# Kernel optimization log

Hardware: AMD Instinct MI355X
Metric: run time of the kernel (lower is better)

The kernel has to match this reference:

```python
import jax, jax.numpy as jnp
import numpy as np

D_MODEL = 768
H = 12
D_K = D_MODEL // H
B = 2
S = 2048
NEG = -1e9


def setup_inputs() -> dict:
    key = jax.random.key(0)
    ks = jax.random.split(key, 12)
    scale = 1.0 / np.sqrt(D_MODEL)
    inp = {
        "q": jax.random.normal(ks[0], (B, S, D_MODEL), jnp.float32),
        "k": jax.random.normal(ks[1], (B, S, D_MODEL), jnp.float32),
        "v": jax.random.normal(ks[2], (B, S, D_MODEL), jnp.float32),
        "mask": jax.random.randint(ks[3], (B, 1, S, S), 0, 2, jnp.int32),
        "Wq": jax.random.normal(ks[4], (D_MODEL, D_MODEL), jnp.float32) * scale,
        "bq": jnp.zeros((D_MODEL,), jnp.float32),
        "Wk": jax.random.normal(ks[5], (D_MODEL, D_MODEL), jnp.float32) * scale,
        "bk": jnp.zeros((D_MODEL,), jnp.float32),
        "Wv": jax.random.normal(ks[6], (D_MODEL, D_MODEL), jnp.float32) * scale,
        "bv": jnp.zeros((D_MODEL,), jnp.float32),
        "Wo": jax.random.normal(ks[7], (D_MODEL, D_MODEL), jnp.float32) * scale,
        "bo": jnp.zeros((D_MODEL,), jnp.float32),
    }
    return inp


def _split_heads(x):
    # [B, S, D] -> [B, H, S, D_K]
    b, s, _ = x.shape
    return x.reshape(b, s, H, D_K).transpose(0, 2, 1, 3)


def reference(q, k, v, mask, Wq, bq, Wk, bk, Wv, bv, Wo, bo):
    # torch Linear: x @ W.T + b
    query = _split_heads(q @ Wq.T + bq)
    key_ = _split_heads(k @ Wk.T + bk)
    value = _split_heads(v @ Wv.T + bv)

    scores = jnp.einsum("bhqd,bhkd->bhqk", query, key_) / np.sqrt(D_K)
    scores = jnp.where(mask == 0, NEG, scores)
    attn = jax.nn.softmax(scores, axis=-1)  # dropout p=0.0 -> identity

    x = jnp.einsum("bhqk,bhkd->bhqd", attn, value)
    x = x.transpose(0, 2, 1, 3).reshape(q.shape[0], -1, D_MODEL)
    return x @ Wo.T + bo
```

## Files before the change

### kernel.cpp

```cpp
#include <hip/hip_runtime.h>
#include <math.h>

#define DMODEL 768
#define NHEAD 12
#define DKDIM 64
#define BB 2
#define SS 2048
#define MROWS (BB * SS)
#define WELEM (DMODEL * DMODEL)
#define MWORDS (SS / 64)
#define NIT (SS / 64)

typedef unsigned short bf16_t;
typedef __attribute__((ext_vector_type(8))) short s8;
typedef __attribute__((ext_vector_type(4))) float f4;

#define MFMA(a, b, c) __builtin_amdgcn_mfma_f32_16x16x32_bf16((a), (b), (c), 0, 0, 0)

__device__ __forceinline__ bf16_t f2bf(float f) {
    unsigned u = __float_as_uint(f);
    u += 0x7fffu + ((u >> 16) & 1u);
    return (bf16_t)(u >> 16);
}
__device__ __forceinline__ unsigned cvtpk2(float a, float b) {
    unsigned r;
    asm("v_cvt_pk_bf16_f32 %0, %1, %2" : "=v"(r) : "v"(a), "v"(b));
    return r;
}
__device__ __forceinline__ s8 ldfrag(const bf16_t* p) {
    union { uint4 u; s8 s; } x;
    x.u = *(const uint4*)p;
    return x.s;
}
__device__ __forceinline__ void gload16(const bf16_t* g, bf16_t* l) {
    __builtin_amdgcn_global_load_lds(
        (__attribute__((address_space(1))) void*)g,
        (__attribute__((address_space(3))) void*)l,
        16, 0, 0);
}

__device__ __forceinline__ void ld_stage(const bf16_t* p, uint4& u0, uint4& u1) {
    u0 = *(const uint4*)p;
    u1 = *(const uint4*)(p + 8);
}

__global__ void cvt_weights(const float* __restrict__ W0, const float* __restrict__ W1,
                            const float* __restrict__ W2, const float* __restrict__ W3,
                            bf16_t* __restrict__ dst)
{
    const float* src = (blockIdx.y == 0) ? W0 : (blockIdx.y == 1) ? W1
                     : (blockIdx.y == 2) ? W2 : W3;
    bf16_t* d = dst + (size_t)blockIdx.y * WELEM;
    const int i = (blockIdx.x * 256 + threadIdx.x) * 4;
    const float4 v = *(const float4*)(src + i);
    ushort4 h;
    h.x = f2bf(v.x); h.y = f2bf(v.y); h.z = f2bf(v.z); h.w = f2bf(v.w);
    *(ushort4*)(d + i) = h;
}

__global__ __launch_bounds__(256) void cvt_inputs(
    const float* __restrict__ A0, const float* __restrict__ A1,
    const float* __restrict__ A2, bf16_t* __restrict__ dst)
{
    const float* src = (blockIdx.y == 0) ? A0 : (blockIdx.y == 1) ? A1 : A2;
    bf16_t* d = dst + (size_t)blockIdx.y * MROWS * DMODEL;
    const int i = (blockIdx.x * 256 + threadIdx.x) * 4;
    const float4 v = *(const float4*)(src + i);
    ushort4 h;
    h.x = f2bf(v.x); h.y = f2bf(v.y); h.z = f2bf(v.z); h.w = f2bf(v.w);
    *(ushort4*)(d + i) = h;
}

__global__ __launch_bounds__(256) void mask_to_bits(
    const int* __restrict__ mask, unsigned long long* __restrict__ mbits)
{
    const size_t gid = (size_t)blockIdx.x * 256 + threadIdx.x;
    const int m = mask[gid];
    const unsigned long long bal = __ballot(m != 0);
    if ((threadIdx.x & 63) == 0) mbits[gid >> 6] = bal;
}

__global__ __launch_bounds__(256) void gemm_qkv(
    const bf16_t* __restrict__ A0, const bf16_t* __restrict__ A1, const bf16_t* __restrict__ A2,
    const bf16_t* __restrict__ W0, const bf16_t* __restrict__ W1, const bf16_t* __restrict__ W2,
    const float* __restrict__ bias0, const float* __restrict__ bias1, const float* __restrict__ bias2,
    bf16_t* __restrict__ C0, bf16_t* __restrict__ C1, bf16_t* __restrict__ C2,
    float sc0, float sc1, float sc2)
{
    __shared__ uint4 As4[128 * 4];
    __shared__ uint4 Bs4[128 * 4];

    const int z = blockIdx.z;
    const bf16_t* A    = (z == 0) ? A0 : (z == 1) ? A1 : A2;
    const bf16_t* W    = (z == 0) ? W0 : (z == 1) ? W1 : W2;
    const float*  bias = (z == 0) ? bias0 : (z == 1) ? bias1 : bias2;
    bf16_t*       C    = (z == 0) ? C0 : (z == 1) ? C1 : C2;
    const float   sc   = (z == 0) ? sc0 : (z == 1) ? sc1 : sc2;

    const int tid  = threadIdx.x;
    const int lane = tid & 63;
    const int w    = tid >> 6;
    const int wm   = w & 1;
    const int wn   = w >> 1;
    const int l15  = lane & 15;
    const int quad = lane >> 4;
    const int m0   = blockIdx.y * 128;
    const int n0   = blockIdx.x * 128;

    const int r0 = tid >> 2,         s0 = (tid & 3) ^ (r0 & 3);
    const int r1 = 64 + (tid >> 2),  s1 = (tid & 3) ^ (r1 & 3);
    const bf16_t* aS0 = A + (size_t)(m0 + r0) * DMODEL + s0 * 8;
    const bf16_t* aS1 = A + (size_t)(m0 + r1) * DMODEL + s1 * 8;
    const bf16_t* wS0 = W + (size_t)(n0 + r0) * DMODEL + s0 * 8;
    const bf16_t* wS1 = W + (size_t)(n0 + r1) * DMODEL + s1 * 8;
    bf16_t* aD0 = (bf16_t*)As4 + w * 512;
    bf16_t* aD1 = (bf16_t*)As4 + 2048 + w * 512;
    bf16_t* bD0 = (bf16_t*)Bs4 + w * 512;
    bf16_t* bD1 = (bf16_t*)Bs4 + 2048 + w * 512;

    f4 acc[4][4];
    #pragma unroll
    for (int i = 0; i < 4; i++)
        #pragma unroll
        for (int j = 0; j < 4; j++)
            acc[i][j] = (f4){0.f, 0.f, 0.f, 0.f};

    for (int k0 = 0; k0 < DMODEL; k0 += 32) {
        __syncthreads();
        gload16(aS0 + k0, aD0);
        gload16(aS1 + k0, aD1);
        gload16(wS0 + k0, bD0);
        gload16(wS1 + k0, bD1);
        __syncthreads();

        s8 af[4], bf[4];
        #pragma unroll
        for (int t = 0; t < 4; t++) {
            const int ar = wm * 64 + t * 16 + l15;
            const int br = wn * 64 + t * 16 + l15;
            union { uint4 u; s8 s; } xa, xb;
            xa.u = As4[ar * 4 + (quad ^ (ar & 3))];
            xb.u = Bs4[br * 4 + (quad ^ (br & 3))];
            af[t] = xa.s;
            bf[t] = xb.s;
        }
        #pragma unroll
        for (int mt = 0; mt < 4; mt++)
            #pragma unroll
            for (int nt = 0; nt < 4; nt++)
                acc[mt][nt] = MFMA(af[mt], bf[nt], acc[mt][nt]);
    }

    #pragma unroll
    for (int mt = 0; mt < 4; mt++) {
        #pragma unroll
        for (int nt = 0; nt < 4; nt++) {
            const int col = n0 + wn * 64 + nt * 16 + l15;
            const float bb = bias[col];
            #pragma unroll
            for (int reg = 0; reg < 4; reg++) {
                const int row = m0 + wm * 64 + mt * 16 + quad * 4 + reg;
                C[(size_t)row * DMODEL + col] = f2bf((acc[mt][nt][reg] + bb) * sc);
            }
        }
    }
}

__global__ __launch_bounds__(256) void gemm_out(
    const bf16_t* __restrict__ A, const bf16_t* __restrict__ W,
    const float* __restrict__ bias, float* __restrict__ C)
{
    __shared__ uint4 As4[64 * 4];
    __shared__ uint4 Bs4[128 * 4];

    const int tid  = threadIdx.x;
    const int lane = tid & 63;
    const int w    = tid >> 6;
    const int l15  = lane & 15;
    const int quad = lane >> 4;
    const int m0   = blockIdx.y * 64;
    const int n0   = blockIdx.x * 128;

    const int srow  = tid >> 1;
    const int shalf = tid & 1;
    const int sw    = srow & 3;
    const int arow  = (tid < 128) ? srow : 0;

    const bf16_t* aptr = A + (size_t)(m0 + arow) * DMODEL + shalf * 16;
    const bf16_t* wptr = W + (size_t)(n0 + srow) * DMODEL + shalf * 16;

    f4 acc[4][2];
    #pragma unroll
    for (int i = 0; i < 4; i++)
        #pragma unroll
        for (int j = 0; j < 2; j++)
            acc[i][j] = (f4){0.f, 0.f, 0.f, 0.f};

    for (int k0 = 0; k0 < DMODEL; k0 += 32) {
        uint4 au0, au1, bu0, bu1;
        if (tid < 128) ld_stage(aptr + k0, au0, au1);
        ld_stage(wptr + k0, bu0, bu1);
        __syncthreads();
        if (tid < 128) {
            As4[srow * 4 + ((shalf * 2 + 0) ^ sw)] = au0;
            As4[srow * 4 + ((shalf * 2 + 1) ^ sw)] = au1;
        }
        Bs4[srow * 4 + ((shalf * 2 + 0) ^ sw)] = bu0;
        Bs4[srow * 4 + ((shalf * 2 + 1) ^ sw)] = bu1;
        __syncthreads();

        s8 af[4], bf[2];
        #pragma unroll
        for (int t = 0; t < 4; t++) {
            const int ar = t * 16 + l15;
            union { uint4 u; s8 s; } xa;
            xa.u = As4[ar * 4 + (quad ^ (ar & 3))];
            af[t] = xa.s;
        }
        #pragma unroll
        for (int nt = 0; nt < 2; nt++) {
            const int br = w * 32 + nt * 16 + l15;
            union { uint4 u; s8 s; } xb;
            xb.u = Bs4[br * 4 + (quad ^ (br & 3))];
            bf[nt] = xb.s;
        }
        #pragma unroll
        for (int mt = 0; mt < 4; mt++)
            #pragma unroll
            for (int nt = 0; nt < 2; nt++)
                acc[mt][nt] = MFMA(af[mt], bf[nt], acc[mt][nt]);
    }

    #pragma unroll
    for (int mt = 0; mt < 4; mt++) {
        #pragma unroll
        for (int nt = 0; nt < 2; nt++) {
            const int col = n0 + w * 32 + nt * 16 + l15;
            const float bb = bias[col];
            #pragma unroll
            for (int reg = 0; reg < 4; reg++) {
                const int row = m0 + mt * 16 + quad * 4 + reg;
                C[(size_t)row * DMODEL + col] = acc[mt][nt][reg] + bb;
            }
        }
    }
}

__global__ __launch_bounds__(256) void attn_mfma(
    const bf16_t* __restrict__ Q, const bf16_t* __restrict__ K,
    const bf16_t* __restrict__ V, const unsigned long long* __restrict__ mbits,
    bf16_t* __restrict__ O)
{
    __shared__ unsigned Vs[2][64][36];

    const int tid  = threadIdx.x;
    const int lane = tid & 63;
    const int w    = tid >> 6;
    const int l15  = lane & 15;
    const int quad = lane >> 4;
    const int q0   = blockIdx.x * 64;
    const int h    = blockIdx.y;
    const int b    = blockIdx.z;
    const size_t base = ((size_t)b * SS) * DMODEL + (size_t)h * DKDIM;

    const bf16_t* qrow = Q + base + (size_t)(q0 + w * 16 + l15) * DMODEL + quad * 8;
    const s8 qf0 = ldfrag(qrow);
    const s8 qf1 = ldfrag(qrow + 32);

    f4 oacc[4];
    #pragma unroll
    for (int i = 0; i < 4; i++) oacc[i] = (f4){0.f, 0.f, 0.f, 0.f};
    float l_part = 0.0f;

    const int kp  = tid & 31;
    const int oct = tid >> 5;
    const bf16_t* vbase = V + base + (size_t)(2 * kp) * DMODEL + oct * 8;
    const bf16_t* kbase = K + base + (size_t)l15 * DMODEL + quad * 8;

    const unsigned long long* mbase =
        mbits + ((size_t)b * SS + (q0 + w * 16 + l15)) * MWORDS;

    const int sA  = l15 + (((2 * quad) & 3) << 4);
    const int sB  = l15 + (((2 * quad + 1) & 3) << 4);
    const bool hiQ = (quad & 2) != 0;

    uint4 va = *(const uint4*)(vbase);
    uint4 vb = *(const uint4*)(vbase + DMODEL);
    {
        const unsigned short* pa = (const unsigned short*)&va;
        const unsigned short* pb = (const unsigned short*)&vb;
        #pragma unroll
        for (int i = 0; i < 8; i++)
            Vs[0][oct * 8 + i][kp] = (unsigned)pa[i] | ((unsigned)pb[i] << 16);
    }
    va = *(const uint4*)(vbase + (size_t)64 * DMODEL);
    vb = *(const uint4*)(vbase + (size_t)64 * DMODEL + DMODEL);

    s8 kf0[4], kf1[4];
    unsigned long long mw;
    #pragma unroll
    for (int nt = 0; nt < 4; nt++) {
        const bf16_t* krow = kbase + (size_t)(nt * 16) * DMODEL;
        kf0[nt] = ldfrag(krow);
        kf1[nt] = ldfrag(krow + 32);
    }
    mw = mbase[0];

    __syncthreads();

    for (int it = 0; it < NIT; ++it) {
        const int k0  = it * 64;
        const int cur = it & 1;

        if (it + 1 < NIT) {
            const unsigned short* pa = (const unsigned short*)&va;
            const unsigned short* pb = (const unsigned short*)&vb;
            #pragma unroll
            for (int i = 0; i < 8; i++)
                Vs[cur ^ 1][oct * 8 + i][kp] = (unsigned)pa[i] | ((unsigned)pb[i] << 16);
            if (it + 2 < NIT) {
                va = *(const uint4*)(vbase + (size_t)(k0 + 128) * DMODEL);
                vb = *(const uint4*)(vbase + (size_t)(k0 + 128) * DMODEL + DMODEL);
            }
        }

        f4 sacc[4];
        __builtin_amdgcn_s_setprio(1);
        #pragma unroll
        for (int nt = 0; nt < 4; nt++) {
            f4 zz = {0.f, 0.f, 0.f, 0.f};
            zz = MFMA(kf0[nt], qf0, zz);
            zz = MFMA(kf1[nt], qf1, zz);
            sacc[nt] = zz;
        }
        __builtin_amdgcn_s_setprio(0);

        const unsigned long long mwc = mw;
        if (it + 1 < NIT) {
            #pragma unroll
            for (int nt = 0; nt < 4; nt++) {
                const bf16_t* krow = kbase + (size_t)(k0 + 64 + nt * 16) * DMODEL;
                kf0[nt] = ldfrag(krow);
                kf1[nt] = ldfrag(krow + 32);
            }
            mw = mbase[it + 1];
        }

        const unsigned ml = ((unsigned)mwc) >> (quad * 4);
        const unsigned mh = ((unsigned)(mwc >> 32)) >> (quad * 4);
        unsigned wlo[4], whi[4];
        #pragma unroll
        for (int nt = 0; nt < 4; nt++) {
            const unsigned mm = (nt & 2) ? mh : ml;
            const int shft = (nt & 1) * 16;
            const float p0 = ((mm >> (shft + 0)) & 1u) ? __builtin_exp2f(sacc[nt][0]) : 0.0f;
            const float p1 = ((mm >> (shft + 1)) & 1u) ? __builtin_exp2f(sacc[nt][1]) : 0.0f;
            const float p2 = ((mm >> (shft + 2)) & 1u) ? __builtin_exp2f(sacc[nt][2]) : 0.0f;
            const float p3 = ((mm >> (shft + 3)) & 1u) ? __builtin_exp2f(sacc[nt][3]) : 0.0f;
            l_part += (p0 + p1) + (p2 + p3);
            wlo[nt] = cvtpk2(p0, p1);
            whi[nt] = cvtpk2(p2, p3);
        }

        #pragma unroll
        for (int kt = 0; kt < 2; kt++) {
            const unsigned a0 = (unsigned)__shfl((int)wlo[2 * kt],     sA, 64);
            const unsigned a1 = (unsigned)__shfl((int)wlo[2 * kt + 1], sA, 64);
            const unsigned b0 = (unsigned)__shfl((int)whi[2 * kt],     sA, 64);
            const unsigned b1 = (unsigned)__shfl((int)whi[2 * kt + 1], sA, 64);
            const unsigned c0 = (unsigned)__shfl((int)wlo[2 * kt],     sB, 64);
            const unsigned c1 = (unsigned)__shfl((int)wlo[2 * kt + 1], sB, 64);
            const unsigned d0 = (unsigned)__shfl((int)whi[2 * kt],     sB, 64);
            const unsigned d1 = (unsigned)__shfl((int)whi[2 * kt + 1], sB, 64);
            union { uint4 u; s8 s; } pf;
            pf.u.x = hiQ ? a1 : a0;
            pf.u.y = hiQ ? b1 : b0;
            pf.u.z = hiQ ? c1 : c0;
            pf.u.w = hiQ ? d1 : d0;

            __builtin_amdgcn_s_setprio(1);
            #pragma unroll
            for (int dt = 0; dt < 4; dt++) {
                union { uint4 u; s8 s; } vf;
                vf.u = *(const uint4*)&Vs[cur][dt * 16 + l15][kt * 16 + quad * 4];
                oacc[dt] = MFMA(pf.s, vf.s, oacc[dt]);
            }
            __builtin_amdgcn_s_setprio(0);
        }

        __syncthreads();
    }

    l_part += __shfl_xor(l_part, 16, 64);
    l_part += __shfl_xor(l_part, 32, 64);
    const float inv = 1.0f / l_part;

    #pragma unroll
    for (int reg = 0; reg < 4; reg++) {
        const float invq = __shfl(inv, (quad << 4) + quad * 4 + reg, 64);
        const size_t row = q0 + w * 16 + quad * 4 + reg;
        #pragma unroll
        for (int dt = 0; dt < 4; dt++) {
            O[base + row * DMODEL + dt * 16 + l15] = f2bf(oacc[dt][reg] * invq);
        }
    }
}

extern "C" void kernel_launch(void* const* d_in, const int* in_sizes, int n_in,
                              void* d_out, int out_size, void* d_ws, size_t ws_size,
                              hipStream_t stream)
{
    const float* q    = (const float*)d_in[0];
    const float* k    = (const float*)d_in[1];
    const float* v    = (const float*)d_in[2];
    const int*   mask = (const int*)  d_in[3];
    const float* Wq   = (const float*)d_in[4];
    const float* bq   = (const float*)d_in[5];
    const float* Wk   = (const float*)d_in[6];
    const float* bk   = (const float*)d_in[7];
    const float* Wv   = (const float*)d_in[8];
    const float* bv   = (const float*)d_in[9];
    const float* Wo   = (const float*)d_in[10];
    const float* bo   = (const float*)d_in[11];
    float* out = (float*)d_out;

    bf16_t* wsb = (bf16_t*)d_ws;
    const size_t plane = (size_t)MROWS * DMODEL;
    bf16_t* Qp  = wsb;
    bf16_t* Kp  = wsb + plane;
    bf16_t* Vp  = wsb + 2 * plane;
    bf16_t* Ctx = wsb + 3 * plane;
    bf16_t* Wqb = wsb + 4 * plane;
    bf16_t* Wkb = Wqb + WELEM;
    bf16_t* Wvb = Wkb + WELEM;
    bf16_t* Wob = Wvb + WELEM;
    bf16_t* Abf = Wob + WELEM;
    unsigned long long* mbits = (unsigned long long*)(Abf + 3 * plane);

    cvt_weights<<<dim3(WELEM / 1024, 4), 256, 0, stream>>>(Wq, Wk, Wv, Wo, Wqb);
    cvt_inputs<<<dim3((int)(plane / 1024), 3), 256, 0, stream>>>(q, k, v, Abf);
    mask_to_bits<<<dim3((BB * SS * SS) / 256), 256, 0, stream>>>(mask, mbits);

    gemm_qkv<<<dim3(DMODEL / 128, MROWS / 128, 3), 256, 0, stream>>>(
        Abf, Abf + plane, Abf + 2 * plane, Wqb, Wkb, Wvb, bq, bk, bv,
        Qp, Kp, Vp, 0.125f * 1.44269504f, 1.0f, 1.0f);

    attn_mfma<<<dim3(SS / 64, NHEAD, BB), 256, 0, stream>>>(Qp, Kp, Vp, mbits, Ctx);

    gemm_out<<<dim3(DMODEL / 128, MROWS / 64), 256, 0, stream>>>(Ctx, Wob, bo, out);
}
```

Baseline: 307.6 us.

## Write V transposed from projection GEMM and split attention keys across two wave groups

The V projection epilogue now writes V in a per-head transposed layout [B,H,DK,S], so the attention kernel can load V fragments straight from global memory into registers. That removes the LDS staging and repacking of V and the per-iteration block barrier. The attention block grows to 512 threads: two groups of four waves each process half of the key range, and their partial outputs and row sums are combined through shared memory at the end. This doubles the waves working on each query tile, at the cost of strided 4-byte stores in the V epilogue and a final reduction step.

```diff
diff --git a/kernel.cpp b/kernel.cpp
--- a/kernel.cpp
+++ b/kernel.cpp
@@ -9,7 +9,8 @@
 #define MROWS (BB * SS)
 #define WELEM (DMODEL * DMODEL)
 #define MWORDS (SS / 64)
-#define NIT (SS / 64)
+#define KCHUNK (SS / 2)
+#define NITH (KCHUNK / 64)
 
 typedef unsigned short bf16_t;
 typedef __attribute__((ext_vector_type(8))) short s8;
@@ -21,6 +22,9 @@
     unsigned u = __float_as_uint(f);
     u += 0x7fffu + ((u >> 16) & 1u);
     return (bf16_t)(u >> 16);
+}
+__device__ __forceinline__ unsigned pack2(float a, float b) {
+    return (unsigned)f2bf(a) | ((unsigned)f2bf(b) << 16);
 }
 __device__ __forceinline__ unsigned cvtpk2(float a, float b) {
     unsigned r;
@@ -153,14 +157,28 @@
 
     #pragma unroll
     for (int mt = 0; mt < 4; mt++) {
+        const int grow = m0 + wm * 64 + mt * 16 + quad * 4;
         #pragma unroll
         for (int nt = 0; nt < 4; nt++) {
             const int col = n0 + wn * 64 + nt * 16 + l15;
             const float bb = bias[col];
-            #pragma unroll
-            for (int reg = 0; reg < 4; reg++) {
-                const int row = m0 + wm * 64 + mt * 16 + quad * 4 + reg;
-                C[(size_t)row * DMODEL + col] = f2bf((acc[mt][nt][reg] + bb) * sc);
+            if (z == 2) {
+                const int bidx = grow >> 11;
+                const int sr   = grow & (SS - 1);
+                const float v0 = acc[mt][nt][0] + bb;
+                const float v1 = acc[mt][nt][1] + bb;
+                const float v2 = acc[mt][nt][2] + bb;
+                const float v3 = acc[mt][nt][3] + bb;
+                unsigned* dst = (unsigned*)(C +
+                    ((size_t)(bidx * NHEAD + (col >> 6)) * DKDIM + (col & 63)) * SS + sr);
+                dst[0] = pack2(v0, v1);
+                dst[1] = pack2(v2, v3);
+            } else {
+                #pragma unroll
+                for (int reg = 0; reg < 4; reg++) {
+                    C[(size_t)(grow + reg) * DMODEL + col] =
+                        f2bf((acc[mt][nt][reg] + bb) * sc);
+                }
             }
         }
     }
@@ -246,24 +264,29 @@
     }
 }
 
-__global__ __launch_bounds__(256) void attn_mfma(
+__global__ __launch_bounds__(512) void attn_mfma(
     const bf16_t* __restrict__ Q, const bf16_t* __restrict__ K,
-    const bf16_t* __restrict__ V, const unsigned long long* __restrict__ mbits,
+    const bf16_t* __restrict__ Vt, const unsigned long long* __restrict__ mbits,
     bf16_t* __restrict__ O)
 {
-    __shared__ unsigned Vs[2][64][36];
+    __shared__ float Osh[4][16][68];
+    __shared__ float Lsh[4][16];
 
     const int tid  = threadIdx.x;
     const int lane = tid & 63;
     const int w    = tid >> 6;
+    const int wq   = w & 3;
+    const int ws   = w >> 2;
     const int l15  = lane & 15;
     const int quad = lane >> 4;
     const int q0   = blockIdx.x * 64;
     const int h    = blockIdx.y;
     const int b    = blockIdx.z;
+    const int ks   = ws * KCHUNK;
     const size_t base = ((size_t)b * SS) * DMODEL + (size_t)h * DKDIM;
-
-    const bf16_t* qrow = Q + base + (size_t)(q0 + w * 16 + l15) * DMODEL + quad * 8;
+    const bf16_t* vtb = Vt + (size_t)(b * NHEAD + h) * DKDIM * SS;
+
+    const bf16_t* qrow = Q + base + (size_t)(q0 + wq * 16 + l15) * DMODEL + quad * 8;
     const s8 qf0 = ldfrag(qrow);
     const s8 qf1 = ldfrag(qrow + 32);
 
@@ -272,57 +295,33 @@
     for (int i = 0; i < 4; i++) oacc[i] = (f4){0.f, 0.f, 0.f, 0.f};
     float l_part = 0.0f;
 
-    const int kp  = tid & 31;
-    const int oct = tid >> 5;
-    const bf16_t* vbase = V + base + (size_t)(2 * kp) * DMODEL + oct * 8;
     const bf16_t* kbase = K + base + (size_t)l15 * DMODEL + quad * 8;
+    const bf16_t* vfb = vtb + (size_t)l15 * SS + ks + quad * 8;
 
     const unsigned long long* mbase =
-        mbits + ((size_t)b * SS + (q0 + w * 16 + l15)) * MWORDS;
+        mbits + ((size_t)b * SS + (q0 + wq * 16 + l15)) * MWORDS + (ks >> 6);
 
     const int sA  = l15 + (((2 * quad) & 3) << 4);
     const int sB  = l15 + (((2 * quad + 1) & 3) << 4);
     const bool hiQ = (quad & 2) != 0;
 
-    uint4 va = *(const uint4*)(vbase);
-    uint4 vb = *(const uint4*)(vbase + DMODEL);
-    {
-        const unsigned short* pa = (const unsigned short*)&va;
-        const unsigned short* pb = (const unsigned short*)&vb;
-        #pragma unroll
-        for (int i = 0; i < 8; i++)
-            Vs[0][oct * 8 + i][kp] = (unsigned)pa[i] | ((unsigned)pb[i] << 16);
-    }
-    va = *(const uint4*)(vbase + (size_t)64 * DMODEL);
-    vb = *(const uint4*)(vbase + (size_t)64 * DMODEL + DMODEL);
-
-    s8 kf0[4], kf1[4];
+    s8 kf0[4], kf1[4], vf0[4], vf1[4];
     unsigned long long mw;
     #pragma unroll
     for (int nt = 0; nt < 4; nt++) {
-        const bf16_t* krow = kbase + (size_t)(nt * 16) * DMODEL;
+        const bf16_t* krow = kbase + (size_t)(ks + nt * 16) * DMODEL;
         kf0[nt] = ldfrag(krow);
         kf1[nt] = ldfrag(krow + 32);
     }
     mw = mbase[0];
-
-    __syncthreads();
-
-    for (int it = 0; it < NIT; ++it) {
-        const int k0  = it * 64;
-        const int cur = it & 1;
-
-        if (it + 1 < NIT) {
-            const unsigned short* pa = (const unsigned short*)&va;
-            const unsigned short* pb = (const unsigned short*)&vb;
-            #pragma unroll
-            for (int i = 0; i < 8; i++)
-                Vs[cur ^ 1][oct * 8 + i][kp] = (unsigned)pa[i] | ((unsigned)pb[i] << 16);
-            if (it + 2 < NIT) {
-                va = *(const uint4*)(vbase + (size_t)(k0 + 128) * DMODEL);
-                vb = *(const uint4*)(vbase + (size_t)(k0 + 128) * DMODEL + DMODEL);
-            }
-        }
+    #pragma unroll
+    for (int dt = 0; dt < 4; dt++) {
+        vf0[dt] = ldfrag(vfb + (size_t)(dt * 16) * SS);
+        vf1[dt] = ldfrag(vfb + (size_t)(dt * 16) * SS + 32);
+    }
+
+    for (int it = 0; it < NITH; ++it) {
+        const int k0 = ks + it * 64;
 
         f4 sacc[4];
         __builtin_amdgcn_s_setprio(1);
@@ -336,7 +335,7 @@
         __builtin_amdgcn_s_setprio(0);
 
         const unsigned long long mwc = mw;
-        if (it + 1 < NIT) {
+        if (it + 1 < NITH) {
             #pragma unroll
             for (int nt = 0; nt < 4; nt++) {
                 const bf16_t* krow = kbase + (size_t)(k0 + 64 + nt * 16) * DMODEL;
@@ -379,29 +378,56 @@
             pf.u.w = hiQ ? d1 : d0;
 
             __builtin_amdgcn_s_setprio(1);
+            if (kt == 0) {
+                #pragma unroll
+                for (int dt = 0; dt < 4; dt++)
+                    oacc[dt] = MFMA(pf.s, vf0[dt], oacc[dt]);
+            } else {
+                #pragma unroll
+                for (int dt = 0; dt < 4; dt++)
+                    oacc[dt] = MFMA(pf.s, vf1[dt], oacc[dt]);
+            }
+            __builtin_amdgcn_s_setprio(0);
+        }
+
+        if (it + 1 < NITH) {
             #pragma unroll
             for (int dt = 0; dt < 4; dt++) {
-                union { uint4 u; s8 s; } vf;
-                vf.u = *(const uint4*)&Vs[cur][dt * 16 + l15][kt * 16 + quad * 4];
-                oacc[dt] = MFMA(pf.s, vf.s, oacc[dt]);
-            }
-            __builtin_amdgcn_s_setprio(0);
-        }
-
-        __syncthreads();
+                vf0[dt] = ldfrag(vfb + (size_t)(dt * 16) * SS + (it + 1) * 64);
+                vf1[dt] = ldfrag(vfb + (size_t)(dt * 16) * SS + (it + 1) * 64 + 32);
+            }
+        }
     }
 
     l_part += __shfl_xor(l_part, 16, 64);
     l_part += __shfl_xor(l_part, 32, 64);
-    const float inv = 1.0f / l_part;
-
-    #pragma unroll
-    for (int reg = 0; reg < 4; reg++) {
-        const float invq = __shfl(inv, (quad << 4) + quad * 4 + reg, 64);
-        const size_t row = q0 + w * 16 + quad * 4 + reg;
-        #pragma unroll
-        for (int dt = 0; dt < 4; dt++) {
-            O[base + row * DMODEL + dt * 16 + l15] = f2bf(oacc[dt][reg] * invq);
+
+    if (ws == 1) {
+        #pragma unroll
+        for (int dt = 0; dt < 4; dt++)
+            #pragma unroll
+            for (int reg = 0; reg < 4; reg++)
+                Osh[wq][quad * 4 + reg][dt * 16 + l15] = oacc[dt][reg];
+        if (quad == 0) Lsh[wq][l15] = l_part;
+    }
+    __syncthreads();
+
+    if (ws == 0) {
+        const float inv = 1.0f / (l_part + Lsh[wq][l15]);
+        #pragma unroll
+        for (int dt = 0; dt < 4; dt++)
+            #pragma unroll
+            for (int reg = 0; reg < 4; reg++)
+                oacc[dt][reg] += Osh[wq][quad * 4 + reg][dt * 16 + l15];
+
+        #pragma unroll
+        for (int reg = 0; reg < 4; reg++) {
+            const float invq = __shfl(inv, (quad << 4) + quad * 4 + reg, 64);
+            const size_t row = q0 + wq * 16 + quad * 4 + reg;
+            #pragma unroll
+            for (int dt = 0; dt < 4; dt++) {
+                O[base + row * DMODEL + dt * 16 + l15] = f2bf(oacc[dt][reg] * invq);
+            }
         }
     }
 }
@@ -428,7 +454,7 @@
     const size_t plane = (size_t)MROWS * DMODEL;
     bf16_t* Qp  = wsb;
     bf16_t* Kp  = wsb + plane;
-    bf16_t* Vp  = wsb + 2 * plane;
+    bf16_t* Vtp = wsb + 2 * plane;
     bf16_t* Ctx = wsb + 3 * plane;
     bf16_t* Wqb = wsb + 4 * plane;
     bf16_t* Wkb = Wqb + WELEM;
@@ -443,9 +469,9 @@
 
     gemm_qkv<<<dim3(DMODEL / 128, MROWS / 128, 3), 256, 0, stream>>>(
         Abf, Abf + plane, Abf + 2 * plane, Wqb, Wkb, Wvb, bq, bk, bv,
-        Qp, Kp, Vp, 0.125f * 1.44269504f, 1.0f, 1.0f);
-
-    attn_mfma<<<dim3(SS / 64, NHEAD, BB), 256, 0, stream>>>(Qp, Kp, Vp, mbits, Ctx);
+        Qp, Kp, Vtp, 0.125f * 1.44269504f, 1.0f, 1.0f);
+
+    attn_mfma<<<dim3(SS / 64, NHEAD, BB), 512, 0, stream>>>(Qp, Kp, Vtp, mbits, Ctx);
 
     gemm_out<<<dim3(DMODEL / 128, MROWS / 64), 256, 0, stream>>>(Ctx, Wob, bo, out);
 }
```

Measured after the change: 381.1 us. +23.9%, slower.
